# Kernel tuning notes

Hardware: AMD Instinct MI355X
Metric: run time of the kernel (lower is better)

Reference implementation:

```python
import jax, jax.numpy as jnp
import numpy as np

B, T, D, H = 4, 2048, 1024, 16
DH = D // H

def setup_inputs() -> dict:
    key = jax.random.key(0)
    k1, k2, k3 = jax.random.split(key, 3)
    x = jax.random.normal(k1, (B, T, D), dtype=jnp.float32)
    w_qkv = jax.random.normal(k2, (D, 3 * D), dtype=jnp.float32) * (1.0 / np.sqrt(D))
    w_out = jax.random.normal(k3, (D, D), dtype=jnp.float32) * (1.0 / np.sqrt(D))
    return {"x": x, "w_qkv": w_qkv, "w_out": w_out}

def reference(x, w_qkv, w_out):
    Bq, Tq, C = x.shape
    qkv = x @ w_qkv                                   # [B,T,3D]
    q, k, v = jnp.split(qkv, 3, axis=-1)
    q = q.reshape(Bq, Tq, H, DH).transpose(0, 2, 1, 3)  # [B,H,T,dh]
    k = k.reshape(Bq, Tq, H, DH).transpose(0, 2, 1, 3)
    v = v.reshape(Bq, Tq, H, DH).transpose(0, 2, 1, 3)
    scores = jnp.einsum('bhqd,bhkd->bhqk', q, k) / jnp.sqrt(jnp.float32(DH))
    mask = jnp.tril(jnp.ones((Tq, Tq), dtype=bool))
    scores = jnp.where(mask, scores, jnp.float32(-jnp.inf))
    attn = jax.nn.softmax(scores, axis=-1)
    out = jnp.einsum('bhqk,bhkd->bhqd', attn, v)      # [B,H,T,dh]
    out = out.transpose(0, 2, 1, 3).reshape(Bq, Tq, C)
    return out @ w_out
```

## Files before the change

kernel.cpp:

```cpp
#include <hip/hip_runtime.h>

#define B_ 4
#define T_ 2048
#define D_ 1024
#define H_ 16
#define DH_ 64
#define BH_ (B_*H_)
#define M_ (B_*T_)
#define N3_ (3*D_)

typedef __attribute__((ext_vector_type(8))) __bf16 bf16x8;
typedef __attribute__((ext_vector_type(4))) float f32x4;
typedef __attribute__((ext_vector_type(16))) float f32x16;
typedef __attribute__((ext_vector_type(8))) unsigned short u16x8;
typedef __attribute__((ext_vector_type(4))) unsigned short u16x4;
typedef int i32x2 __attribute__((ext_vector_type(2)));

__device__ inline void gload_lds16(const void* g, void* l) {
  __builtin_amdgcn_global_load_lds((const __attribute__((address_space(1))) void*)g,
                                   (__attribute__((address_space(3))) void*)l, 16, 0, 0);
}

__device__ inline unsigned short f2bf(float v) {
  __bf16 t = (__bf16)v;
  return *(unsigned short*)&t;
}

__device__ inline unsigned pk2(float lo, float hi2) {
  return (unsigned)f2bf(lo) | ((unsigned)f2bf(hi2) << 16);
}

template<int BASE>
__device__ inline bf16x8 buildP(const f32x16& S) {
  unsigned a = pk2(S[BASE+0], S[BASE+1]);
  unsigned b = pk2(S[BASE+2], S[BASE+3]);
  unsigned c = pk2(S[BASE+4], S[BASE+5]);
  unsigned d = pk2(S[BASE+6], S[BASE+7]);
  i32x2 r0 = __builtin_amdgcn_permlane32_swap((int)a, (int)c, false, false);
  i32x2 r1 = __builtin_amdgcn_permlane32_swap((int)b, (int)d, false, false);
  union { unsigned u[4]; bf16x8 v; } U;
  U.u[0] = (unsigned)r0[0];
  U.u[1] = (unsigned)r1[0];
  U.u[2] = (unsigned)r0[1];
  U.u[3] = (unsigned)r1[1];
  return U.v;
}

__global__ void prep(const float* __restrict__ x, unsigned short* __restrict__ xb,
                     const float* __restrict__ wq, unsigned short* __restrict__ wqT,
                     const float* __restrict__ wo, unsigned short* __restrict__ woT) {
  __shared__ unsigned short lds[64][72];
  int bid = blockIdx.x, tid = threadIdx.x;
  if (bid < 4096) {
    int i = bid * 256 + tid;
    const float4* p = (const float4*)(x + (size_t)i * 8);
    float4 a = p[0], b = p[1];
    float v[8] = {a.x, a.y, a.z, a.w, b.x, b.y, b.z, b.w};
    u16x8 r;
#pragma unroll
    for (int j = 0; j < 8; ++j) r[j] = f2bf(v[j]);
    *(u16x8*)(xb + (size_t)i * 8) = r;
    return;
  }
  const float* w;
  unsigned short* wt;
  int n0, k0, Ndim;
  if (bid < 4096 + 768) {
    int b2 = bid - 4096;
    w = wq; wt = wqT; Ndim = N3_;
    n0 = (b2 % 48) * 64; k0 = (b2 / 48) * 64;
  } else {
    int b3 = bid - 4864;
    w = wo; wt = woT; Ndim = D_;
    n0 = (b3 % 16) * 64; k0 = (b3 / 16) * 64;
  }
#pragma unroll
  for (int i = 0; i < 2; ++i) {
    int idx = i * 256 + tid;
    int r = idx >> 3, c8 = idx & 7;
    const float4* src = (const float4*)(w + (size_t)(k0 + r) * Ndim + n0 + c8 * 8);
    float4 a = src[0], b = src[1];
    float v[8] = {a.x, a.y, a.z, a.w, b.x, b.y, b.z, b.w};
#pragma unroll
    for (int j = 0; j < 8; ++j) lds[r][c8 * 8 + j] = f2bf(v[j]);
  }
  __syncthreads();
#pragma unroll
  for (int i = 0; i < 2; ++i) {
    int idx = i * 256 + tid;
    int r = idx >> 3, c8 = idx & 7;
    u16x8 o;
#pragma unroll
    for (int j = 0; j < 8; ++j) o[j] = lds[c8 * 8 + j][r];
    *(u16x8*)(wt + (size_t)(n0 + r) * 1024 + k0 + c8 * 8) = o;
  }
}

__global__ __launch_bounds__(256) void gemm2b(
    const unsigned short* __restrict__ A,
    const unsigned short* __restrict__ BT,
    int epi,
    unsigned short* __restrict__ qb, unsigned short* __restrict__ kb, unsigned short* __restrict__ vtb,
    float* __restrict__ outf) {
  extern __shared__ __align__(16) char lds[];
  const int tid = threadIdx.x;
  const int wave = tid >> 6, lane = tid & 63, g = lane >> 4, c = lane & 15;
  const int wm = wave >> 1, wn = wave & 1;
  int flat = blockIdx.y * gridDim.x + blockIdx.x;
  int xcd = flat & 7, local = flat >> 3;
  int bx = xcd * 8 + (local & 7);
  int by = local >> 3;
  const int m0 = bx * 128, n0 = by * 128;

  f32x4 acc[4][4] = {};

  auto stage = [&](int slot, int jj) {
    char* sb = lds + slot * 32768;
#pragma unroll
    for (int i = 0; i < 4; ++i) {
      int idx = i * 256 + tid;
      int r = idx >> 3, s = idx & 7;
      gload_lds16(A + (size_t)(m0 + r) * 1024 + jj * 64 + 8 * (s ^ (r & 7)),
                  sb + idx * 16);
    }
#pragma unroll
    for (int i = 0; i < 4; ++i) {
      int idx = i * 256 + tid;
      int r = idx >> 3, s = idx & 7;
      gload_lds16(BT + (size_t)(n0 + r) * 1024 + jj * 64 + 8 * (s ^ (r & 7)),
                  sb + 16384 + idx * 16);
    }
  };

  stage(0, 0);
  for (int j = 0; j < 16; ++j) {
    if (j < 15) {
      stage((j + 1) & 1, j + 1);
      asm volatile("s_waitcnt vmcnt(8)" ::: "memory");
    } else {
      asm volatile("s_waitcnt vmcnt(0)" ::: "memory");
    }
    __builtin_amdgcn_s_barrier();
    asm volatile("" ::: "memory");

    const char* sA = lds + (j & 1) * 32768;
    const char* sB = sA + 16384;
#pragma unroll
    for (int kc = 0; kc < 2; ++kc) {
      bf16x8 af[4], bf[4];
#pragma unroll
      for (int mt = 0; mt < 4; ++mt) {
        int r = wm * 64 + mt * 16 + c;
        af[mt] = *(const bf16x8*)(sA + r * 128 + 16 * ((kc * 4 + g) ^ (r & 7)));
      }
#pragma unroll
      for (int nt = 0; nt < 4; ++nt) {
        int r = wn * 64 + nt * 16 + c;
        bf[nt] = *(const bf16x8*)(sB + r * 128 + 16 * ((kc * 4 + g) ^ (r & 7)));
      }
      __builtin_amdgcn_s_setprio(1);
#pragma unroll
      for (int mt = 0; mt < 4; ++mt)
#pragma unroll
        for (int nt = 0; nt < 4; ++nt)
          acc[mt][nt] = __builtin_amdgcn_mfma_f32_16x16x32_bf16(af[mt], bf[nt], acc[mt][nt], 0, 0, 0);
      __builtin_amdgcn_s_setprio(0);
    }

    __builtin_amdgcn_s_barrier();
    asm volatile("" ::: "memory");
  }

  if (epi == 0) {
    int which = n0 >> 10;
    int colbase = n0 - (which << 10);
    if (which == 2) {
#pragma unroll
      for (int mt = 0; mt < 4; ++mt)
#pragma unroll
        for (int nt = 0; nt < 4; ++nt) {
          int m = m0 + wm * 64 + mt * 16 + g * 4;
          int n = colbase + wn * 64 + nt * 16 + c;
          int b = m >> 11, t = m & 2047;
          int h = n >> 6, d = n & 63;
          u16x4 pk;
#pragma unroll
          for (int i = 0; i < 4; ++i) pk[i] = f2bf(acc[mt][nt][i]);
          *(u16x4*)(vtb + ((size_t)(b * H_ + h) * 64 + d) * T_ + t) = pk;
        }
    } else {
      unsigned short* dst = which == 0 ? qb : kb;
      float scale = which == 0 ? 0.18033688011112042f : 1.0f;
#pragma unroll
      for (int mt = 0; mt < 4; ++mt)
#pragma unroll
        for (int nt = 0; nt < 4; ++nt)
#pragma unroll
          for (int i = 0; i < 4; ++i) {
            int m = m0 + wm * 64 + mt * 16 + g * 4 + i;
            int n = colbase + wn * 64 + nt * 16 + c;
            int b = m >> 11, t = m & 2047;
            int h = n >> 6, d = n & 63;
            dst[(((size_t)(b * H_ + h) * T_ + t) << 6) + d] = f2bf(acc[mt][nt][i] * scale);
          }
    }
  } else {
#pragma unroll
    for (int mt = 0; mt < 4; ++mt)
#pragma unroll
      for (int nt = 0; nt < 4; ++nt)
#pragma unroll
        for (int i = 0; i < 4; ++i) {
          int m = m0 + wm * 64 + mt * 16 + g * 4 + i;
          int n = n0 + wn * 64 + nt * 16 + c;
          outf[(size_t)m * 1024 + n] = acc[mt][nt][i];
        }
  }
}

#define PV_STEP(PF, KC)                                                                \
  {                                                                                    \
    bf16x8 pf = (PF);                                                                  \
    int dr0 = q32, dr1 = 32 + q32;                                                     \
    bf16x8 v0 = *(const bf16x8*)(sV + dr0 * 128 + 16 * (((KC)*2 + hi) ^ (dr0 & 7)));   \
    bf16x8 v1 = *(const bf16x8*)(sV + dr1 * 128 + 16 * (((KC)*2 + hi) ^ (dr1 & 7)));   \
    oT0 = __builtin_amdgcn_mfma_f32_32x32x16_bf16(v0, pf, oT0, 0, 0, 0);               \
    oT1 = __builtin_amdgcn_mfma_f32_32x32x16_bf16(v1, pf, oT1, 0, 0, 0);               \
  }

__global__ __launch_bounds__(512) void attn(
    const unsigned short* __restrict__ qbp,
    const unsigned short* __restrict__ kb,
    const unsigned short* __restrict__ vt,
    unsigned short* __restrict__ ao) {
  __shared__ __align__(16) char pool[65536];
  const int tid = threadIdx.x;
  const int wave = tid >> 6, lane = tid & 63;
  const int q32 = lane & 31, hi = lane >> 5;
  const int bh = blockIdx.y;
  const int flip = (bh >> 5) & 1;
  const int pb = flip ? blockIdx.x : (T_ / 256 - 1) - blockIdx.x;
  const int q0w = pb * 256 + wave * 32;
  const int kmax = 4 * pb + 3;
  const int dtile = 4 * pb + (wave >> 1);

  bf16x8 qf[4];
#pragma unroll
  for (int dhc = 0; dhc < 4; ++dhc)
    qf[dhc] = *(const bf16x8*)(qbp + ((size_t)bh * T_ + q0w + q32) * 64 + dhc * 16 + hi * 8);

  f32x16 oT0 = {}, oT1 = {};
  float l_run = 0.0f;

  auto stage = [&](int buf, int kt) {
    int r = tid >> 3, s8 = tid & 7;
    gload_lds16(kb + ((size_t)bh * T_ + kt * 64 + r) * 64 + 8 * (s8 ^ (r & 7)),
                pool + buf * 16384 + tid * 16);
    gload_lds16(vt + ((size_t)bh * 64 + r) * T_ + kt * 64 + 8 * (s8 ^ (r & 7)),
                pool + buf * 16384 + 8192 + tid * 16);
  };

  stage(0, 0);
  stage(1, 1);
  stage(2, 2);
  for (int kt = 0; kt <= kmax; ++kt) {
    if (kt + 2 <= kmax)      { asm volatile("s_waitcnt vmcnt(4)" ::: "memory"); }
    else if (kt + 1 <= kmax) { asm volatile("s_waitcnt vmcnt(2)" ::: "memory"); }
    else                     { asm volatile("s_waitcnt vmcnt(0)" ::: "memory"); }
    __builtin_amdgcn_s_barrier();
    asm volatile("" ::: "memory");
    if (kt + 3 <= kmax) stage((kt + 3) & 3, kt + 3);
    if (kt <= dtile) {
      const char* sK = pool + (kt & 3) * 16384;
      const char* sV = sK + 8192;

      f32x16 st0 = {}, st1 = {};
      __builtin_amdgcn_s_setprio(1);
#pragma unroll
      for (int dhc = 0; dhc < 4; ++dhc) {
        int kr0 = q32, kr1 = 32 + q32;
        bf16x8 k0 = *(const bf16x8*)(sK + kr0 * 128 + 16 * ((dhc * 2 + hi) ^ (kr0 & 7)));
        bf16x8 k1 = *(const bf16x8*)(sK + kr1 * 128 + 16 * ((dhc * 2 + hi) ^ (kr1 & 7)));
        st0 = __builtin_amdgcn_mfma_f32_32x32x16_bf16(k0, qf[dhc], st0, 0, 0, 0);
        st1 = __builtin_amdgcn_mfma_f32_32x32x16_bf16(k1, qf[dhc], st1, 0, 0, 0);
      }
      __builtin_amdgcn_s_setprio(0);

      if (kt == dtile) {
        int qg = q0w + q32;
#pragma unroll
        for (int r = 0; r < 16; ++r) {
          int krow = kt * 64 + (r & 3) + 8 * (r >> 2) + 4 * hi;
          if (krow > qg) st0[r] = -INFINITY;
          if (krow + 32 > qg) st1[r] = -INFINITY;
        }
      }

      float ps0 = 0.0f, ps1 = 0.0f, ps2 = 0.0f, ps3 = 0.0f;
#pragma unroll
      for (int r = 0; r < 16; r += 4) {
        float a0 = __builtin_amdgcn_exp2f(st0[r + 0]); st0[r + 0] = a0; ps0 += a0;
        float a1 = __builtin_amdgcn_exp2f(st0[r + 1]); st0[r + 1] = a1; ps1 += a1;
        float a2 = __builtin_amdgcn_exp2f(st0[r + 2]); st0[r + 2] = a2; ps2 += a2;
        float a3 = __builtin_amdgcn_exp2f(st0[r + 3]); st0[r + 3] = a3; ps3 += a3;
      }
#pragma unroll
      for (int r = 0; r < 16; r += 4) {
        float a0 = __builtin_amdgcn_exp2f(st1[r + 0]); st1[r + 0] = a0; ps0 += a0;
        float a1 = __builtin_amdgcn_exp2f(st1[r + 1]); st1[r + 1] = a1; ps1 += a1;
        float a2 = __builtin_amdgcn_exp2f(st1[r + 2]); st1[r + 2] = a2; ps2 += a2;
        float a3 = __builtin_amdgcn_exp2f(st1[r + 3]); st1[r + 3] = a3; ps3 += a3;
      }
      float ps = (ps0 + ps1) + (ps2 + ps3);
      ps += __shfl_xor(ps, 32);
      l_run += ps;

      __builtin_amdgcn_s_setprio(1);
      PV_STEP(buildP<0>(st0), 0)
      PV_STEP(buildP<8>(st0), 1)
      PV_STEP(buildP<0>(st1), 2)
      PV_STEP(buildP<8>(st1), 3)
      __builtin_amdgcn_s_setprio(0);
    }
  }

  __syncthreads();
  unsigned short* ep = (unsigned short*)pool + wave * (32 * 72);
  float inv_l = 1.0f / l_run;
#pragma unroll
  for (int r = 0; r < 16; ++r) {
    int d0 = (r & 3) + 8 * (r >> 2) + 4 * hi;
    ep[q32 * 72 + d0]      = f2bf(oT0[r] * inv_l);
    ep[q32 * 72 + 32 + d0] = f2bf(oT1[r] * inv_l);
  }
  __syncthreads();
  {
    int q = lane >> 1, half = lane & 1;
    int t = q0w + q;
    int b = bh >> 4, h = bh & 15;
    const unsigned short* row = ep + q * 72 + half * 32;
    unsigned short* g = ao + ((size_t)(b * T_ + t)) * 1024 + h * 64 + half * 32;
#pragma unroll
    for (int j = 0; j < 4; ++j)
      *(u16x8*)(g + j * 8) = *(const u16x8*)(row + j * 8);
  }
}

extern "C" void kernel_launch(void* const* d_in, const int* in_sizes, int n_in,
                              void* d_out, int out_size, void* d_ws, size_t ws_size,
                              hipStream_t stream) {
  const float* x = (const float*)d_in[0];
  const float* w_qkv = (const float*)d_in[1];
  const float* w_out = (const float*)d_in[2];
  float* out = (float*)d_out;

  char* ws = (char*)d_ws;
  size_t off = 0;
  auto alloc = [&](size_t bytes) {
    char* p = ws + off;
    off += (bytes + 255) & ~(size_t)255;
    return p;
  };
  unsigned short* xb    = (unsigned short*)alloc((size_t)M_ * D_ * 2);
  unsigned short* wqkvT = (unsigned short*)alloc((size_t)N3_ * D_ * 2);
  unsigned short* woutT = (unsigned short*)alloc((size_t)D_ * D_ * 2);
  unsigned short* qbuf  = (unsigned short*)alloc((size_t)BH_ * T_ * 64 * 2);
  unsigned short* kbuf  = (unsigned short*)alloc((size_t)BH_ * T_ * 64 * 2);
  unsigned short* vtb   = (unsigned short*)alloc((size_t)BH_ * 64 * T_ * 2);
  unsigned short* ao    = xb;

  hipFuncSetAttribute(reinterpret_cast<const void*>(gemm2b),
                      hipFuncAttributeMaxDynamicSharedMemorySize, 65536);

  prep<<<4096 + 768 + 256, 256, 0, stream>>>(x, xb, w_qkv, wqkvT, w_out, woutT);
  gemm2b<<<dim3(M_ / 128, N3_ / 128), 256, 65536, stream>>>(xb, wqkvT, 0, qbuf, kbuf, vtb, nullptr);
  attn<<<dim3(T_ / 256, BH_), 512, 0, stream>>>(qbuf, kbuf, vtb, ao);
  gemm2b<<<dim3(M_ / 128, D_ / 128), 256, 65536, stream>>>(ao, woutT, 1, nullptr, nullptr, nullptr, out);
}
```

Baseline: 148.7 us.

## Shrink attention blocks to 4 waves with double-buffered K/V staging

```diff
diff --git a/kernel.cpp b/kernel.cpp
--- a/kernel.cpp
+++ b/kernel.cpp
@@ -228,21 +228,21 @@
     oT1 = __builtin_amdgcn_mfma_f32_32x32x16_bf16(v1, pf, oT1, 0, 0, 0);               \
   }
 
-__global__ __launch_bounds__(512) void attn(
+__global__ __launch_bounds__(256) void attn(
     const unsigned short* __restrict__ qbp,
     const unsigned short* __restrict__ kb,
     const unsigned short* __restrict__ vt,
     unsigned short* __restrict__ ao) {
-  __shared__ __align__(16) char pool[65536];
+  __shared__ __align__(16) char pool[32768];
   const int tid = threadIdx.x;
   const int wave = tid >> 6, lane = tid & 63;
   const int q32 = lane & 31, hi = lane >> 5;
   const int bh = blockIdx.y;
-  const int flip = (bh >> 5) & 1;
-  const int pb = flip ? blockIdx.x : (T_ / 256 - 1) - blockIdx.x;
-  const int q0w = pb * 256 + wave * 32;
-  const int kmax = 4 * pb + 3;
-  const int dtile = 4 * pb + (wave >> 1);
+  const int flip = (bh >> 4) & 1;
+  const int pb = flip ? blockIdx.x : (T_ / 128 - 1) - blockIdx.x;
+  const int q0w = pb * 128 + wave * 32;
+  const int kmax = 2 * pb + 1;
+  const int dtile = 2 * pb + (wave >> 1);
 
   bf16x8 qf[4];
 #pragma unroll
@@ -253,25 +253,34 @@
   float l_run = 0.0f;
 
   auto stage = [&](int buf, int kt) {
-    int r = tid >> 3, s8 = tid & 7;
-    gload_lds16(kb + ((size_t)bh * T_ + kt * 64 + r) * 64 + 8 * (s8 ^ (r & 7)),
-                pool + buf * 16384 + tid * 16);
-    gload_lds16(vt + ((size_t)bh * 64 + r) * T_ + kt * 64 + 8 * (s8 ^ (r & 7)),
-                pool + buf * 16384 + 8192 + tid * 16);
+#pragma unroll
+    for (int i = 0; i < 2; ++i) {
+      int idx = i * 256 + tid;
+      int r = idx >> 3, s8 = idx & 7;
+      gload_lds16(kb + ((size_t)bh * T_ + kt * 64 + r) * 64 + 8 * (s8 ^ (r & 7)),
+                  pool + buf * 16384 + idx * 16);
+    }
+#pragma unroll
+    for (int i = 0; i < 2; ++i) {
+      int idx = i * 256 + tid;
+      int r = idx >> 3, s8 = idx & 7;
+      gload_lds16(vt + ((size_t)bh * 64 + r) * T_ + kt * 64 + 8 * (s8 ^ (r & 7)),
+                  pool + buf * 16384 + 8192 + idx * 16);
+    }
   };
 
   stage(0, 0);
-  stage(1, 1);
-  stage(2, 2);
   for (int kt = 0; kt <= kmax; ++kt) {
-    if (kt + 2 <= kmax)      { asm volatile("s_waitcnt vmcnt(4)" ::: "memory"); }
-    else if (kt + 1 <= kmax) { asm volatile("s_waitcnt vmcnt(2)" ::: "memory"); }
-    else                     { asm volatile("s_waitcnt vmcnt(0)" ::: "memory"); }
+    if (kt < kmax) {
+      stage((kt + 1) & 1, kt + 1);
+      asm volatile("s_waitcnt vmcnt(4)" ::: "memory");
+    } else {
+      asm volatile("s_waitcnt vmcnt(0)" ::: "memory");
+    }
     __builtin_amdgcn_s_barrier();
     asm volatile("" ::: "memory");
-    if (kt + 3 <= kmax) stage((kt + 3) & 3, kt + 3);
     if (kt <= dtile) {
-      const char* sK = pool + (kt & 3) * 16384;
+      const char* sK = pool + (kt & 1) * 16384;
       const char* sV = sK + 8192;
 
       f32x16 st0 = {}, st1 = {};
@@ -322,9 +331,10 @@
       PV_STEP(buildP<8>(st1), 3)
       __builtin_amdgcn_s_setprio(0);
     }
-  }
-
-  __syncthreads();
+    __builtin_amdgcn_s_barrier();
+    asm volatile("" ::: "memory");
+  }
+
   unsigned short* ep = (unsigned short*)pool + wave * (32 * 72);
   float inv_l = 1.0f / l_run;
 #pragma unroll
@@ -374,6 +384,6 @@
 
   prep<<<4096 + 768 + 256, 256, 0, stream>>>(x, xb, w_qkv, wqkvT, w_out, woutT);
   gemm2b<<<dim3(M_ / 128, N3_ / 128), 256, 65536, stream>>>(xb, wqkvT, 0, qbuf, kbuf, vtb, nullptr);
-  attn<<<dim3(T_ / 256, BH_), 512, 0, stream>>>(qbuf, kbuf, vtb, ao);
+  attn<<<dim3(T_ / 128, BH_), 256, 0, stream>>>(qbuf, kbuf, vtb, ao);
   gemm2b<<<dim3(M_ / 128, D_ / 128), 256, 65536, stream>>>(ao, woutT, 1, nullptr, nullptr, nullptr, out);
 }
```

Result: slower. 169.4 us (+13.9%).
